# Optimization experiments

Hardware: AMD Instinct MI355X
Metric: run time of the kernel (lower is better)

## Reference

```python
import jax, jax.numpy as jnp
import numpy as np


def _fro(x):
    # torch.norm(x, 2) on a matrix flattens -> Frobenius norm
    return jnp.sqrt(jnp.sum(x * x))


def _torch_median(x):
    # torch.median returns the lower of the two middle values for even counts
    f = jnp.sort(x.reshape(-1))
    return f[(f.shape[0] - 1) // 2]


def setup_inputs() -> dict:
    key = jax.random.key(0)
    ks = jax.random.split(key, 6)
    return {
        "c2": jax.random.normal(ks[0], (100, 128, 56, 56), dtype=jnp.float32),
        "c3": jax.random.normal(ks[1], (100, 256, 28, 28), dtype=jnp.float32),
        "vmask1": jax.random.normal(ks[2], (100, 128), dtype=jnp.float32),
        "vmask2": jax.random.normal(ks[3], (100, 256), dtype=jnp.float32),
        "amask1": jax.random.normal(ks[4], (100, 128), dtype=jnp.float32),
        "amask2": jax.random.normal(ks[5], (100, 256), dtype=jnp.float32),
    }


def reference(c2, c3, vmask1, vmask2, amask1, amask2):
    # Vectorized equivalent of the 100x128 / 100x256 scalar-copy loops
    tm1 = c2[:, :, 7, 7]  # [100, 128]
    tm2 = c3[:, :, 3, 3]  # [100, 256]

    p = (_fro(tm1 - vmask1) + _fro(tm2 - vmask2)) / (12800.0 + 25600.0)

    c2m = _torch_median(tm1)
    c3m = _torch_median(tm2)
    b1 = jnp.where(tm1 < c2m, 0.0, 1.0).astype(tm1.dtype)
    b2 = jnp.where(tm2 < c3m, 0.0, 1.0).astype(tm2.dtype)

    q = (_fro(b1 - amask1) + _fro(b2 - amask2)) / (128.0 + 256.0)

    return jnp.stack([p, q])  # [2]: (p, q)
```

## Files before the change

kernel.cpp:

```cpp
#include <hip/hip_runtime.h>
#include <math.h>


#define N1 12800
#define N2 25600
#define K1 6399
#define K2 12799
#define NBINS 4096
#define HSHIFT 20
#define CAP 1024

__device__ __forceinline__ unsigned fkey(float f) {
    unsigned u = __float_as_uint(f);
    return (u & 0x80000000u) ? ~u : (u | 0x80000000u);
}

__device__ __forceinline__ float block_reduce(float v, float* red) {
    const int lane = threadIdx.x & 63;
    const int wid  = threadIdx.x >> 6;
    const int nw   = (blockDim.x + 63) >> 6;
#pragma unroll
    for (int o = 32; o > 0; o >>= 1) v += __shfl_down(v, o, 64);
    if (lane == 0) red[wid] = v;
    __syncthreads();
    if (wid == 0) {
        v = (lane < nw) ? red[lane] : 0.f;
#pragma unroll
        for (int o = 8; o > 0; o >>= 1) v += __shfl_down(v, o, 64);
    }
    __syncthreads();
    return v;
}

__global__ __launch_bounds__(256) void gather_kernel(
    const float* __restrict__ c2, const float* __restrict__ c3,
    const float* __restrict__ vm1, const float* __restrict__ vm2,
    const float* __restrict__ am1, const float* __restrict__ am2,
    float* __restrict__ W1, float* __restrict__ W2,
    float* __restrict__ partialP, float* __restrict__ partialA2,
    unsigned* __restrict__ hist1, unsigned* __restrict__ hist2,
    float* __restrict__ T1, float* __restrict__ T2)
{
    __shared__ float red[16];
    int g = blockIdx.x * 256 + threadIdx.x;
    float d, a;
    if (g < N1) {
        float v = c2[(size_t)g * 3136 + 399];
        W1[g] = v;
        d = v - vm1[g];
        a = am1[g];
        unsigned b = fkey(v) >> HSHIFT;
        atomicAdd(&hist1[b], 1u);
        atomicAdd(&T1[b], 1.f - 2.f * a);
    } else {
        int j = g - N1;
        float v = c3[(size_t)j * 784 + 87];
        W2[j] = v;
        d = v - vm2[j];
        a = am2[j];
        unsigned b = fkey(v) >> HSHIFT;
        atomicAdd(&hist2[b], 1u);
        atomicAdd(&T2[b], 1.f - 2.f * a);
    }
    float pss = block_reduce(d * d, red);
    float ass = block_reduce(a * a, red);
    if (threadIdx.x == 0) {
        partialP[blockIdx.x]  = pss;
        partialA2[blockIdx.x] = ass;
    }
}

__device__ void hist_scan(const unsigned* __restrict__ histg, int k,
                          unsigned* sh_h, unsigned* sh_csum, unsigned* sh_wsum,
                          int* sh_bin, int* sh_kk)
{
    const int t = threadIdx.x;
    __syncthreads();
    for (int i = t; i < NBINS; i += 1024) sh_h[i] = histg[i];
    __syncthreads();
    unsigned c = sh_h[4*t] + sh_h[4*t+1] + sh_h[4*t+2] + sh_h[4*t+3];
    sh_csum[t] = c;
    unsigned wv = c;
#pragma unroll
    for (int o = 32; o > 0; o >>= 1) wv += __shfl_down(wv, o, 64);
    if ((t & 63) == 0) sh_wsum[t >> 6] = wv;
    __syncthreads();
    if (t == 0) {
        int rem = k;
        int w = 0;
        for (; w < 16; ++w) { unsigned s = sh_wsum[w]; if ((unsigned)rem < s) break; rem -= (int)s; }
        int tc = w * 64;
        for (; tc < (w + 1) * 64; ++tc) { unsigned s = sh_csum[tc]; if ((unsigned)rem < s) break; rem -= (int)s; }
        int b = tc * 4;
        for (; b < tc * 4 + 4; ++b) { unsigned s = sh_h[b]; if ((unsigned)rem < s) break; rem -= (int)s; }
        *sh_bin = b;
        *sh_kk  = rem;
    }
    __syncthreads();
}

__device__ void cand_select(const float* __restrict__ W, int n,
                            const float* __restrict__ am,
                            int bin, int kk,
                            unsigned* cand_u, float* cand_a,
                            int* sh_m, unsigned* sh_res, float* red,
                            float* corr)
{
    const int t = threadIdx.x;
    if (t == 0) *sh_m = 0;
    __syncthreads();
    for (int i = t; i < n; i += 1024) {
        unsigned u = fkey(W[i]);
        if ((int)(u >> HSHIFT) == bin) {
            int p = atomicAdd(sh_m, 1);
            if (p < CAP) { cand_u[p] = u; cand_a[p] = am[i]; }
        }
    }
    __syncthreads();
    const int m = (*sh_m < CAP) ? *sh_m : CAP;
    for (int i = t; i < m; i += 1024) {
        unsigned ui = cand_u[i];
        int r = 0;
        for (int j = 0; j < m; ++j) {
            unsigned uj = cand_u[j];
            r += (uj < ui) || (uj == ui && j < i);
        }
        if (r == kk) *sh_res = ui;
    }
    __syncthreads();
    const unsigned um = *sh_res;
    float cc = 0.f;
    for (int i = t; i < m; i += 1024)
        if (cand_u[i] >= um) cc += 1.f - 2.f * cand_a[i];
    float tot = block_reduce(cc, red);
    if (t == 0) *corr = tot;
    __syncthreads();
}

__global__ __launch_bounds__(1024) void finish_kernel(
    const float* __restrict__ W1, const float* __restrict__ W2,
    const float* __restrict__ partialP, const float* __restrict__ partialA2,
    const unsigned* __restrict__ hist1, const unsigned* __restrict__ hist2,
    const float* __restrict__ T1, const float* __restrict__ T2,
    const float* __restrict__ am1, const float* __restrict__ am2,
    float* __restrict__ out)
{
    __shared__ unsigned sh_h[NBINS];
    __shared__ unsigned sh_csum[1024];
    __shared__ unsigned sh_wsum[16];
    __shared__ unsigned cand_u[CAP];
    __shared__ float    cand_a[CAP];
    __shared__ float    red[16];
    __shared__ int sh_bin, sh_kk, sh_m;
    __shared__ unsigned sh_res;
    __shared__ float sh_corr1, sh_corr2;

    const int t = threadIdx.x;

    float s1  = block_reduce((t < 50) ? partialP[t] : 0.f, red);
    float s2  = block_reduce((t >= 50 && t < 150) ? partialP[t] : 0.f, red);
    float a21 = block_reduce((t < 50) ? partialA2[t] : 0.f, red);
    float a22 = block_reduce((t >= 50 && t < 150) ? partialA2[t] : 0.f, red);

    hist_scan(hist1, K1, sh_h, sh_csum, sh_wsum, &sh_bin, &sh_kk);
    int b1 = sh_bin, kk1 = sh_kk;
    float sv = 0.f;
#pragma unroll
    for (int j = 0; j < 4; ++j) { int b = 4*t + j; if (b > b1) sv += T1[b]; }
    float suff1 = block_reduce(sv, red);
    cand_select(W1, N1, am1, b1, kk1, cand_u, cand_a, &sh_m, &sh_res, red, &sh_corr1);

    hist_scan(hist2, K2, sh_h, sh_csum, sh_wsum, &sh_bin, &sh_kk);
    int b2 = sh_bin, kk2 = sh_kk;
    sv = 0.f;
#pragma unroll
    for (int j = 0; j < 4; ++j) { int b = 4*t + j; if (b > b2) sv += T2[b]; }
    float suff2 = block_reduce(sv, red);
    cand_select(W2, N2, am2, b2, kk2, cand_u, cand_a, &sh_m, &sh_res, red, &sh_corr2);

    if (t == 0) {
        float q1 = a21 + suff1 + sh_corr1;
        float q2 = a22 + suff2 + sh_corr2;
        out[0] = (sqrtf(s1) + sqrtf(s2)) / 38400.f;
        out[1] = (sqrtf(q1) + sqrtf(q2)) / 384.f;
    }
}

extern "C" void kernel_launch(void* const* d_in, const int* in_sizes, int n_in,
                              void* d_out, int out_size, void* d_ws, size_t ws_size,
                              hipStream_t stream) {
    const float* c2  = (const float*)d_in[0];
    const float* c3  = (const float*)d_in[1];
    const float* vm1 = (const float*)d_in[2];
    const float* vm2 = (const float*)d_in[3];
    const float* am1 = (const float*)d_in[4];
    const float* am2 = (const float*)d_in[5];
    float* out = (float*)d_out;

    float* ws = (float*)d_ws;
    float* W1        = ws;
    float* W2        = ws + N1;
    float* partialP  = ws + 38400;
    float* partialA2 = ws + 38560;
    unsigned* hist1  = (unsigned*)(ws + 38720);
    unsigned* hist2  = hist1 + NBINS;
    float* T1        = (float*)(hist2 + NBINS);
    float* T2        = T1 + NBINS;

    hipMemsetAsync(hist1, 0, 4 * NBINS * sizeof(unsigned), stream);
    gather_kernel<<<150, 256, 0, stream>>>(c2, c3, vm1, vm2, am1, am2,
                                           W1, W2, partialP, partialA2,
                                           hist1, hist2, T1, T2);
    finish_kernel<<<1, 1024, 0, stream>>>(W1, W2, partialP, partialA2,
                                          hist1, hist2, T1, T2, am1, am2, out);
}
```

Baseline: 283.6 us.

## Fuse memset, gather and median finish into one cooperative kernel

Replaces the memset plus two kernel launches with a single cooperative kernel of 38 blocks. Workspace zeroing, gather, histogramming, histogram scans and candidate collection all run inside it, separated by grid syncs. Candidates are kept from the registers holding the gathered values, so the old single-block rescan of all gathered values is gone and only block 0 does the final rank selection. This removes launch overhead and the serial single-block pass over 38400 elements, at the cost of three grid-wide barriers and every block redundantly scanning both histograms.

```diff
diff --git a/kernel.cpp b/kernel.cpp
--- a/kernel.cpp
+++ b/kernel.cpp
@@ -1,14 +1,19 @@
 #include <hip/hip_runtime.h>
+#include <hip/hip_cooperative_groups.h>
 #include <math.h>
+
+namespace cg = cooperative_groups;
 
 
 #define N1 12800
 #define N2 25600
+#define NTOT 38400
 #define K1 6399
 #define K2 12799
 #define NBINS 4096
 #define HSHIFT 20
 #define CAP 1024
+#define NB 38
 
 __device__ __forceinline__ unsigned fkey(float f) {
     unsigned u = __float_as_uint(f);
@@ -18,56 +23,17 @@
 __device__ __forceinline__ float block_reduce(float v, float* red) {
     const int lane = threadIdx.x & 63;
     const int wid  = threadIdx.x >> 6;
-    const int nw   = (blockDim.x + 63) >> 6;
 #pragma unroll
     for (int o = 32; o > 0; o >>= 1) v += __shfl_down(v, o, 64);
     if (lane == 0) red[wid] = v;
     __syncthreads();
     if (wid == 0) {
-        v = (lane < nw) ? red[lane] : 0.f;
+        v = (lane < 16) ? red[lane] : 0.f;
 #pragma unroll
         for (int o = 8; o > 0; o >>= 1) v += __shfl_down(v, o, 64);
     }
     __syncthreads();
     return v;
-}
-
-__global__ __launch_bounds__(256) void gather_kernel(
-    const float* __restrict__ c2, const float* __restrict__ c3,
-    const float* __restrict__ vm1, const float* __restrict__ vm2,
-    const float* __restrict__ am1, const float* __restrict__ am2,
-    float* __restrict__ W1, float* __restrict__ W2,
-    float* __restrict__ partialP, float* __restrict__ partialA2,
-    unsigned* __restrict__ hist1, unsigned* __restrict__ hist2,
-    float* __restrict__ T1, float* __restrict__ T2)
-{
-    __shared__ float red[16];
-    int g = blockIdx.x * 256 + threadIdx.x;
-    float d, a;
-    if (g < N1) {
-        float v = c2[(size_t)g * 3136 + 399];
-        W1[g] = v;
-        d = v - vm1[g];
-        a = am1[g];
-        unsigned b = fkey(v) >> HSHIFT;
-        atomicAdd(&hist1[b], 1u);
-        atomicAdd(&T1[b], 1.f - 2.f * a);
-    } else {
-        int j = g - N1;
-        float v = c3[(size_t)j * 784 + 87];
-        W2[j] = v;
-        d = v - vm2[j];
-        a = am2[j];
-        unsigned b = fkey(v) >> HSHIFT;
-        atomicAdd(&hist2[b], 1u);
-        atomicAdd(&T2[b], 1.f - 2.f * a);
-    }
-    float pss = block_reduce(d * d, red);
-    float ass = block_reduce(a * a, red);
-    if (threadIdx.x == 0) {
-        partialP[blockIdx.x]  = pss;
-        partialA2[blockIdx.x] = ass;
-    }
 }
 
 __device__ void hist_scan(const unsigned* __restrict__ histg, int k,
@@ -99,88 +65,132 @@
     __syncthreads();
 }
 
-__device__ void cand_select(const float* __restrict__ W, int n,
-                            const float* __restrict__ am,
-                            int bin, int kk,
-                            unsigned* cand_u, float* cand_a,
-                            int* sh_m, unsigned* sh_res, float* red,
-                            float* corr)
+__device__ float cand_corr(const unsigned* __restrict__ gu, const float* __restrict__ ga,
+                           int m, int kk,
+                           unsigned* cu, float* ca, unsigned* sh_res, float* red)
 {
     const int t = threadIdx.x;
-    if (t == 0) *sh_m = 0;
-    __syncthreads();
-    for (int i = t; i < n; i += 1024) {
-        unsigned u = fkey(W[i]);
-        if ((int)(u >> HSHIFT) == bin) {
-            int p = atomicAdd(sh_m, 1);
-            if (p < CAP) { cand_u[p] = u; cand_a[p] = am[i]; }
-        }
-    }
-    __syncthreads();
-    const int m = (*sh_m < CAP) ? *sh_m : CAP;
+    for (int i = t; i < m; i += 1024) { cu[i] = gu[i]; ca[i] = ga[i]; }
+    __syncthreads();
     for (int i = t; i < m; i += 1024) {
-        unsigned ui = cand_u[i];
+        unsigned ui = cu[i];
         int r = 0;
-        for (int j = 0; j < m; ++j) {
-            unsigned uj = cand_u[j];
-            r += (uj < ui) || (uj == ui && j < i);
-        }
+        for (int j = 0; j < m; ++j) { unsigned uj = cu[j]; r += (uj < ui) || (uj == ui && j < i); }
         if (r == kk) *sh_res = ui;
     }
     __syncthreads();
     const unsigned um = *sh_res;
     float cc = 0.f;
     for (int i = t; i < m; i += 1024)
-        if (cand_u[i] >= um) cc += 1.f - 2.f * cand_a[i];
-    float tot = block_reduce(cc, red);
-    if (t == 0) *corr = tot;
-    __syncthreads();
-}
-
-__global__ __launch_bounds__(1024) void finish_kernel(
-    const float* __restrict__ W1, const float* __restrict__ W2,
-    const float* __restrict__ partialP, const float* __restrict__ partialA2,
-    const unsigned* __restrict__ hist1, const unsigned* __restrict__ hist2,
-    const float* __restrict__ T1, const float* __restrict__ T2,
+        if (cu[i] >= um) cc += 1.f - 2.f * ca[i];
+    return block_reduce(cc, red);
+}
+
+__global__ __launch_bounds__(1024) void fused_kernel(
+    const float* __restrict__ c2, const float* __restrict__ c3,
+    const float* __restrict__ vm1, const float* __restrict__ vm2,
     const float* __restrict__ am1, const float* __restrict__ am2,
-    float* __restrict__ out)
+    float* __restrict__ ws, float* __restrict__ out)
 {
+    unsigned* hist1 = (unsigned*)ws;
+    unsigned* hist2 = hist1 + NBINS;
+    float* T1 = ws + 2*NBINS;
+    float* T2 = T1 + NBINS;
+    unsigned* cnts = (unsigned*)(T2 + NBINS);
+    float* pP1 = ws + 16400;
+    float* pP2 = pP1 + 64;
+    float* pA1 = pP2 + 64;
+    float* pA2 = pA1 + 64;
+    unsigned* c1u = (unsigned*)(pA2 + 64);
+    float*    c1a = (float*)(c1u + CAP);
+    unsigned* c2u = (unsigned*)(c1a + CAP);
+    float*    c2a = (float*)(c2u + CAP);
+
     __shared__ unsigned sh_h[NBINS];
     __shared__ unsigned sh_csum[1024];
     __shared__ unsigned sh_wsum[16];
-    __shared__ unsigned cand_u[CAP];
-    __shared__ float    cand_a[CAP];
+    __shared__ unsigned sh_cu[CAP];
+    __shared__ float    sh_ca[CAP];
     __shared__ float    red[16];
-    __shared__ int sh_bin, sh_kk, sh_m;
+    __shared__ int sh_bin, sh_kk;
     __shared__ unsigned sh_res;
-    __shared__ float sh_corr1, sh_corr2;
-
+
+    cg::grid_group grid = cg::this_grid();
     const int t = threadIdx.x;
-
-    float s1  = block_reduce((t < 50) ? partialP[t] : 0.f, red);
-    float s2  = block_reduce((t >= 50 && t < 150) ? partialP[t] : 0.f, red);
-    float a21 = block_reduce((t < 50) ? partialA2[t] : 0.f, red);
-    float a22 = block_reduce((t >= 50 && t < 150) ? partialA2[t] : 0.f, red);
+    const int g = blockIdx.x * 1024 + t;
+    const bool act1 = (g < N1);
+    const bool act2 = (g >= N1) && (g < NTOT);
+
+    float v = 0.f, a = 0.f, d = 0.f;
+    if (act1) {
+        v = c2[(size_t)g * 3136 + 399];
+        a = am1[g];
+        d = v - vm1[g];
+    } else if (act2) {
+        int j = g - N1;
+        v = c3[(size_t)j * 784 + 87];
+        a = am2[j];
+        d = v - vm2[j];
+    }
+
+    if (g < 2*NBINS) ((unsigned*)ws)[g] = 0u;
+    else if (g < 4*NBINS) ws[g] = 0.f;
+    else if (g < 4*NBINS + 2) cnts[g - 4*NBINS] = 0u;
+    grid.sync();
+
+    const unsigned key = fkey(v);
+    const unsigned b = key >> HSHIFT;
+    if (act1) { atomicAdd(&hist1[b], 1u); atomicAdd(&T1[b], 1.f - 2.f * a); }
+    else if (act2) { atomicAdd(&hist2[b], 1u); atomicAdd(&T2[b], 1.f - 2.f * a); }
+    float r;
+    r = block_reduce(act1 ? d * d : 0.f, red);  if (t == 0) pP1[blockIdx.x] = r;
+    r = block_reduce(act2 ? d * d : 0.f, red);  if (t == 0) pP2[blockIdx.x] = r;
+    r = block_reduce(act1 ? a * a : 0.f, red);  if (t == 0) pA1[blockIdx.x] = r;
+    r = block_reduce(act2 ? a * a : 0.f, red);  if (t == 0) pA2[blockIdx.x] = r;
+    grid.sync();
 
     hist_scan(hist1, K1, sh_h, sh_csum, sh_wsum, &sh_bin, &sh_kk);
-    int b1 = sh_bin, kk1 = sh_kk;
-    float sv = 0.f;
-#pragma unroll
-    for (int j = 0; j < 4; ++j) { int b = 4*t + j; if (b > b1) sv += T1[b]; }
-    float suff1 = block_reduce(sv, red);
-    cand_select(W1, N1, am1, b1, kk1, cand_u, cand_a, &sh_m, &sh_res, red, &sh_corr1);
-
+    const int b1 = sh_bin, kk1 = sh_kk;
     hist_scan(hist2, K2, sh_h, sh_csum, sh_wsum, &sh_bin, &sh_kk);
-    int b2 = sh_bin, kk2 = sh_kk;
-    sv = 0.f;
-#pragma unroll
-    for (int j = 0; j < 4; ++j) { int b = 4*t + j; if (b > b2) sv += T2[b]; }
-    float suff2 = block_reduce(sv, red);
-    cand_select(W2, N2, am2, b2, kk2, cand_u, cand_a, &sh_m, &sh_res, red, &sh_corr2);
+    const int b2 = sh_bin, kk2 = sh_kk;
+
+    float suff1 = 0.f, suff2 = 0.f;
+    if (blockIdx.x == 0) {
+        float sv = 0.f;
+#pragma unroll
+        for (int j = 0; j < 4; ++j) { int bb = 4*t + j; if (bb > b1) sv += T1[bb]; }
+        suff1 = block_reduce(sv, red);
+        sv = 0.f;
+#pragma unroll
+        for (int j = 0; j < 4; ++j) { int bb = 4*t + j; if (bb > b2) sv += T2[bb]; }
+        suff2 = block_reduce(sv, red);
+    }
+
+    if (act1 && (int)b == b1) {
+        unsigned p = atomicAdd(&cnts[0], 1u);
+        if (p < CAP) { c1u[p] = key; c1a[p] = a; }
+    }
+    if (act2 && (int)b == b2) {
+        unsigned p = atomicAdd(&cnts[1], 1u);
+        if (p < CAP) { c2u[p] = key; c2a[p] = a; }
+    }
+    grid.sync();
+
+    if (blockIdx.x != 0) return;
+
+    float s1  = block_reduce((t < NB) ? pP1[t] : 0.f, red);
+    float s2  = block_reduce((t < NB) ? pP2[t] : 0.f, red);
+    float a21 = block_reduce((t < NB) ? pA1[t] : 0.f, red);
+    float a22 = block_reduce((t < NB) ? pA2[t] : 0.f, red);
+
+    int m1 = (cnts[0] < (unsigned)CAP) ? (int)cnts[0] : CAP;
+    int m2 = (cnts[1] < (unsigned)CAP) ? (int)cnts[1] : CAP;
+    float corr1 = cand_corr(c1u, c1a, m1, kk1, sh_cu, sh_ca, &sh_res, red);
+    float corr2 = cand_corr(c2u, c2a, m2, kk2, sh_cu, sh_ca, &sh_res, red);
 
     if (t == 0) {
-        float q1 = a21 + suff1 + sh_corr1;
-        float q2 = a22 + suff2 + sh_corr2;
+        float q1 = a21 + suff1 + corr1;
+        float q2 = a22 + suff2 + corr2;
         out[0] = (sqrtf(s1) + sqrtf(s2)) / 38400.f;
         out[1] = (sqrtf(q1) + sqrtf(q2)) / 384.f;
     }
@@ -195,22 +205,10 @@
     const float* vm2 = (const float*)d_in[3];
     const float* am1 = (const float*)d_in[4];
     const float* am2 = (const float*)d_in[5];
+    float* ws  = (float*)d_ws;
     float* out = (float*)d_out;
 
-    float* ws = (float*)d_ws;
-    float* W1        = ws;
-    float* W2        = ws + N1;
-    float* partialP  = ws + 38400;
-    float* partialA2 = ws + 38560;
-    unsigned* hist1  = (unsigned*)(ws + 38720);
-    unsigned* hist2  = hist1 + NBINS;
-    float* T1        = (float*)(hist2 + NBINS);
-    float* T2        = T1 + NBINS;
-
-    hipMemsetAsync(hist1, 0, 4 * NBINS * sizeof(unsigned), stream);
-    gather_kernel<<<150, 256, 0, stream>>>(c2, c3, vm1, vm2, am1, am2,
-                                           W1, W2, partialP, partialA2,
-                                           hist1, hist2, T1, T2);
-    finish_kernel<<<1, 1024, 0, stream>>>(W1, W2, partialP, partialA2,
-                                          hist1, hist2, T1, T2, am1, am2, out);
-}
+    void* args[] = { &c2, &c3, &vm1, &vm2, &am1, &am2, &ws, &out };
+    hipLaunchCooperativeKernel((void*)fused_kernel, dim3(NB), dim3(1024),
+                               args, 0, stream);
+}
```

New measurement: 308.0 us. 8.6% more time.

## Build median histograms in shared memory of finish kernel, drop memset and global atomics

Applied to the files above, without the earlier changes.

The histogram and per-bin amask sums were built with global atomics in the gather kernel, after a memset launch. They are now built with shared-memory atomics inside the single-block finish kernel. The gather kernel stores pre-transformed sort keys, and the finish kernel keeps them in registers, so one pass accumulates the a^2 sum, the above-bin contribution and the candidate collection. This removes a memset launch and contended global atomics, but moves more serial work onto one 1024-thread block.

```diff
diff --git a/kernel.cpp b/kernel.cpp
--- a/kernel.cpp
+++ b/kernel.cpp
@@ -9,22 +9,39 @@
 #define NBINS 4096
 #define HSHIFT 20
 #define CAP 1024
+#define J1 13
+#define J2 25
 
 __device__ __forceinline__ unsigned fkey(float f) {
     unsigned u = __float_as_uint(f);
     return (u & 0x80000000u) ? ~u : (u | 0x80000000u);
 }
 
-__device__ __forceinline__ float block_reduce(float v, float* red) {
+__device__ __forceinline__ float block_reduce256(float v, float* red) {
     const int lane = threadIdx.x & 63;
     const int wid  = threadIdx.x >> 6;
-    const int nw   = (blockDim.x + 63) >> 6;
 #pragma unroll
     for (int o = 32; o > 0; o >>= 1) v += __shfl_down(v, o, 64);
     if (lane == 0) red[wid] = v;
     __syncthreads();
     if (wid == 0) {
-        v = (lane < nw) ? red[lane] : 0.f;
+        v = (lane < 4) ? red[lane] : 0.f;
+        v += __shfl_down(v, 2, 64);
+        v += __shfl_down(v, 1, 64);
+    }
+    __syncthreads();
+    return v;
+}
+
+__device__ __forceinline__ float block_reduce1024(float v, float* red) {
+    const int lane = threadIdx.x & 63;
+    const int wid  = threadIdx.x >> 6;
+#pragma unroll
+    for (int o = 32; o > 0; o >>= 1) v += __shfl_down(v, o, 64);
+    if (lane == 0) red[wid] = v;
+    __syncthreads();
+    if (wid == 0) {
+        v = (lane < 16) ? red[lane] : 0.f;
 #pragma unroll
         for (int o = 8; o > 0; o >>= 1) v += __shfl_down(v, o, 64);
     }
@@ -35,49 +52,54 @@
 __global__ __launch_bounds__(256) void gather_kernel(
     const float* __restrict__ c2, const float* __restrict__ c3,
     const float* __restrict__ vm1, const float* __restrict__ vm2,
-    const float* __restrict__ am1, const float* __restrict__ am2,
-    float* __restrict__ W1, float* __restrict__ W2,
-    float* __restrict__ partialP, float* __restrict__ partialA2,
-    unsigned* __restrict__ hist1, unsigned* __restrict__ hist2,
-    float* __restrict__ T1, float* __restrict__ T2)
+    unsigned* __restrict__ W1, unsigned* __restrict__ W2,
+    float* __restrict__ partialP)
 {
-    __shared__ float red[16];
-    int g = blockIdx.x * 256 + threadIdx.x;
-    float d, a;
+    __shared__ float red[4];
+    const int g = blockIdx.x * 256 + threadIdx.x;
+    float d;
     if (g < N1) {
         float v = c2[(size_t)g * 3136 + 399];
-        W1[g] = v;
+        W1[g] = fkey(v);
         d = v - vm1[g];
-        a = am1[g];
-        unsigned b = fkey(v) >> HSHIFT;
-        atomicAdd(&hist1[b], 1u);
-        atomicAdd(&T1[b], 1.f - 2.f * a);
     } else {
         int j = g - N1;
         float v = c3[(size_t)j * 784 + 87];
-        W2[j] = v;
+        W2[j] = fkey(v);
         d = v - vm2[j];
-        a = am2[j];
-        unsigned b = fkey(v) >> HSHIFT;
-        atomicAdd(&hist2[b], 1u);
-        atomicAdd(&T2[b], 1.f - 2.f * a);
-    }
-    float pss = block_reduce(d * d, red);
-    float ass = block_reduce(a * a, red);
-    if (threadIdx.x == 0) {
-        partialP[blockIdx.x]  = pss;
-        partialA2[blockIdx.x] = ass;
-    }
-}
-
-__device__ void hist_scan(const unsigned* __restrict__ histg, int k,
-                          unsigned* sh_h, unsigned* sh_csum, unsigned* sh_wsum,
-                          int* sh_bin, int* sh_kk)
+    }
+    float pss = block_reduce256(d * d, red);
+    if (threadIdx.x == 0) partialP[blockIdx.x] = pss;
+}
+
+template<int J, int N>
+__device__ float process(const unsigned* __restrict__ Wk,
+                         const float* __restrict__ am, int K,
+                         unsigned* sh_h, unsigned* sh_csum, unsigned* sh_wsum,
+                         unsigned* sh_cu, float* sh_ca, float* red,
+                         int* sh_bin, int* sh_kk, int* sh_m, unsigned* sh_res)
 {
     const int t = threadIdx.x;
-    __syncthreads();
-    for (int i = t; i < NBINS; i += 1024) sh_h[i] = histg[i];
-    __syncthreads();
+
+    __syncthreads();
+    for (int i = t; i < NBINS; i += 1024) sh_h[i] = 0u;
+    if (t == 0) *sh_m = 0;
+    __syncthreads();
+
+    unsigned k[J];
+#pragma unroll
+    for (int j = 0; j < J; ++j) {
+        int i = t + j * 1024;
+        if (i < N) {
+            unsigned u = Wk[i];
+            k[j] = u;
+            atomicAdd(&sh_h[u >> HSHIFT], 1u);
+        } else {
+            k[j] = 0u;
+        }
+    }
+    __syncthreads();
+
     unsigned c = sh_h[4*t] + sh_h[4*t+1] + sh_h[4*t+2] + sh_h[4*t+3];
     sh_csum[t] = c;
     unsigned wv = c;
@@ -86,7 +108,7 @@
     if ((t & 63) == 0) sh_wsum[t >> 6] = wv;
     __syncthreads();
     if (t == 0) {
-        int rem = k;
+        int rem = K;
         int w = 0;
         for (; w < 16; ++w) { unsigned s = sh_wsum[w]; if ((unsigned)rem < s) break; rem -= (int)s; }
         int tc = w * 64;
@@ -97,90 +119,71 @@
         *sh_kk  = rem;
     }
     __syncthreads();
-}
-
-__device__ void cand_select(const float* __restrict__ W, int n,
-                            const float* __restrict__ am,
-                            int bin, int kk,
-                            unsigned* cand_u, float* cand_a,
-                            int* sh_m, unsigned* sh_res, float* red,
-                            float* corr)
-{
-    const int t = threadIdx.x;
-    if (t == 0) *sh_m = 0;
-    __syncthreads();
-    for (int i = t; i < n; i += 1024) {
-        unsigned u = fkey(W[i]);
-        if ((int)(u >> HSHIFT) == bin) {
-            int p = atomicAdd(sh_m, 1);
-            if (p < CAP) { cand_u[p] = u; cand_a[p] = am[i]; }
+    const int bm = *sh_bin, kk = *sh_kk;
+
+    float cc = 0.f;
+#pragma unroll
+    for (int j = 0; j < J; ++j) {
+        int i = t + j * 1024;
+        if (i < N) {
+            float a = am[i];
+            cc += a * a;
+            unsigned u = k[j];
+            int bb = (int)(u >> HSHIFT);
+            if (bb > bm) {
+                cc += 1.f - 2.f * a;
+            } else if (bb == bm) {
+                int p = atomicAdd(sh_m, 1);
+                if (p < CAP) { sh_cu[p] = u; sh_ca[p] = a; }
+            }
         }
     }
     __syncthreads();
     const int m = (*sh_m < CAP) ? *sh_m : CAP;
+
     for (int i = t; i < m; i += 1024) {
-        unsigned ui = cand_u[i];
+        unsigned ui = sh_cu[i];
         int r = 0;
         for (int j = 0; j < m; ++j) {
-            unsigned uj = cand_u[j];
+            unsigned uj = sh_cu[j];
             r += (uj < ui) || (uj == ui && j < i);
         }
         if (r == kk) *sh_res = ui;
     }
     __syncthreads();
     const unsigned um = *sh_res;
-    float cc = 0.f;
     for (int i = t; i < m; i += 1024)
-        if (cand_u[i] >= um) cc += 1.f - 2.f * cand_a[i];
-    float tot = block_reduce(cc, red);
-    if (t == 0) *corr = tot;
-    __syncthreads();
+        if (sh_cu[i] >= um) cc += 1.f - 2.f * sh_ca[i];
+
+    return block_reduce1024(cc, red);
 }
 
 __global__ __launch_bounds__(1024) void finish_kernel(
-    const float* __restrict__ W1, const float* __restrict__ W2,
-    const float* __restrict__ partialP, const float* __restrict__ partialA2,
-    const unsigned* __restrict__ hist1, const unsigned* __restrict__ hist2,
-    const float* __restrict__ T1, const float* __restrict__ T2,
+    const unsigned* __restrict__ W1, const unsigned* __restrict__ W2,
+    const float* __restrict__ partialP,
     const float* __restrict__ am1, const float* __restrict__ am2,
     float* __restrict__ out)
 {
     __shared__ unsigned sh_h[NBINS];
     __shared__ unsigned sh_csum[1024];
     __shared__ unsigned sh_wsum[16];
-    __shared__ unsigned cand_u[CAP];
-    __shared__ float    cand_a[CAP];
+    __shared__ unsigned sh_cu[CAP];
+    __shared__ float    sh_ca[CAP];
     __shared__ float    red[16];
     __shared__ int sh_bin, sh_kk, sh_m;
     __shared__ unsigned sh_res;
-    __shared__ float sh_corr1, sh_corr2;
 
     const int t = threadIdx.x;
 
-    float s1  = block_reduce((t < 50) ? partialP[t] : 0.f, red);
-    float s2  = block_reduce((t >= 50 && t < 150) ? partialP[t] : 0.f, red);
-    float a21 = block_reduce((t < 50) ? partialA2[t] : 0.f, red);
-    float a22 = block_reduce((t >= 50 && t < 150) ? partialA2[t] : 0.f, red);
-
-    hist_scan(hist1, K1, sh_h, sh_csum, sh_wsum, &sh_bin, &sh_kk);
-    int b1 = sh_bin, kk1 = sh_kk;
-    float sv = 0.f;
-#pragma unroll
-    for (int j = 0; j < 4; ++j) { int b = 4*t + j; if (b > b1) sv += T1[b]; }
-    float suff1 = block_reduce(sv, red);
-    cand_select(W1, N1, am1, b1, kk1, cand_u, cand_a, &sh_m, &sh_res, red, &sh_corr1);
-
-    hist_scan(hist2, K2, sh_h, sh_csum, sh_wsum, &sh_bin, &sh_kk);
-    int b2 = sh_bin, kk2 = sh_kk;
-    sv = 0.f;
-#pragma unroll
-    for (int j = 0; j < 4; ++j) { int b = 4*t + j; if (b > b2) sv += T2[b]; }
-    float suff2 = block_reduce(sv, red);
-    cand_select(W2, N2, am2, b2, kk2, cand_u, cand_a, &sh_m, &sh_res, red, &sh_corr2);
+    float s1 = block_reduce1024((t < 50) ? partialP[t] : 0.f, red);
+    float s2 = block_reduce1024((t >= 50 && t < 150) ? partialP[t] : 0.f, red);
+
+    float q1 = process<J1, N1>(W1, am1, K1, sh_h, sh_csum, sh_wsum,
+                               sh_cu, sh_ca, red, &sh_bin, &sh_kk, &sh_m, &sh_res);
+    float q2 = process<J2, N2>(W2, am2, K2, sh_h, sh_csum, sh_wsum,
+                               sh_cu, sh_ca, red, &sh_bin, &sh_kk, &sh_m, &sh_res);
 
     if (t == 0) {
-        float q1 = a21 + suff1 + sh_corr1;
-        float q2 = a22 + suff2 + sh_corr2;
         out[0] = (sqrtf(s1) + sqrtf(s2)) / 38400.f;
         out[1] = (sqrtf(q1) + sqrtf(q2)) / 384.f;
     }
@@ -198,19 +201,10 @@
     float* out = (float*)d_out;
 
     float* ws = (float*)d_ws;
-    float* W1        = ws;
-    float* W2        = ws + N1;
-    float* partialP  = ws + 38400;
-    float* partialA2 = ws + 38560;
-    unsigned* hist1  = (unsigned*)(ws + 38720);
-    unsigned* hist2  = hist1 + NBINS;
-    float* T1        = (float*)(hist2 + NBINS);
-    float* T2        = T1 + NBINS;
-
-    hipMemsetAsync(hist1, 0, 4 * NBINS * sizeof(unsigned), stream);
-    gather_kernel<<<150, 256, 0, stream>>>(c2, c3, vm1, vm2, am1, am2,
-                                           W1, W2, partialP, partialA2,
-                                           hist1, hist2, T1, T2);
-    finish_kernel<<<1, 1024, 0, stream>>>(W1, W2, partialP, partialA2,
-                                          hist1, hist2, T1, T2, am1, am2, out);
-}
+    unsigned* W1       = (unsigned*)ws;
+    unsigned* W2       = W1 + N1;
+    float*    partialP = ws + 38400;
+
+    gather_kernel<<<150, 256, 0, stream>>>(c2, c3, vm1, vm2, W1, W2, partialP);
+    finish_kernel<<<1, 1024, 0, stream>>>(W1, W2, partialP, am1, am2, out);
+}
```

New measurement: 258.2 us. 1.1x faster.
